# Kernel tuning notes

Hardware: AMD Instinct MI355X
Metric: run time of the kernel (lower is better)

The kernel has to match this reference:

```python
import jax, jax.numpy as jnp
import numpy as np

COST_CLASS = 1.0
COST_BBOX = 1.0
COST_GIOU = 1.0


def box_cxcywh_to_xyxy(b):
    cx, cy, w, h = jnp.split(b, 4, axis=-1)
    return jnp.concatenate([cx - 0.5 * w, cy - 0.5 * h, cx + 0.5 * w, cy + 0.5 * h], axis=-1)


def generalized_box_iou(b1, b2):
    # b1: [N,4] xyxy, b2: [M,4] xyxy -> [N,M]
    a1 = (b1[:, 2] - b1[:, 0]) * (b1[:, 3] - b1[:, 1])  # [N]
    a2 = (b2[:, 2] - b2[:, 0]) * (b2[:, 3] - b2[:, 1])  # [M]
    lt = jnp.maximum(b1[:, None, :2], b2[None, :, :2])  # [N,M,2]
    rb = jnp.minimum(b1[:, None, 2:], b2[None, :, 2:])
    wh = jnp.clip(rb - lt, 0.0)
    inter = wh[..., 0] * wh[..., 1]
    union = a1[:, None] + a2[None, :] - inter
    iou = inter / union
    lt_e = jnp.minimum(b1[:, None, :2], b2[None, :, :2])
    rb_e = jnp.maximum(b1[:, None, 2:], b2[None, :, 2:])
    wh_e = jnp.clip(rb_e - lt_e, 0.0)
    area = wh_e[..., 0] * wh_e[..., 1]
    return iou - (area - union) / area


def setup_inputs() -> dict:
    key = jax.random.key(0)
    k1, k2, k3, k4, k5 = jax.random.split(key, 5)
    bs, nq, d, total_tgt = 16, 900, 256, 1600
    return {
        "pred_logits": jax.random.normal(k1, (bs, nq, d), dtype=jnp.float32),
        "pred_boxes": jax.random.uniform(k2, (bs, nq, 4), dtype=jnp.float32),
        "tgt_embs": jax.random.normal(k3, (total_tgt, d), dtype=jnp.float32),
        "tgt_bbox": jax.random.uniform(k4, (total_tgt, 4), dtype=jnp.float32),
        "tgt_sizes": jax.random.randint(k5, (bs,), 0, 100, dtype=jnp.int32),  # only used by host-side LSA
    }


def reference(pred_logits, pred_boxes, tgt_embs, tgt_bbox, tgt_sizes):
    # Returns the sigmoid-squashed cost volume C [bs, num_queries, total_tgt];
    # scipy linear_sum_assignment over tgt_sizes splits is a host-side step.
    bs, nq = pred_logits.shape[:2]
    out_prob = pred_logits.reshape(bs * nq, -1)
    out_bbox = pred_boxes.reshape(bs * nq, 4)
    out_prob = out_prob / jnp.linalg.norm(out_prob, axis=-1, keepdims=True)
    cost_class = jax.nn.relu(out_prob @ tgt_embs.T)                    # [N,M]
    cost_bbox = jnp.sum(jnp.abs(out_bbox[:, None, :] - tgt_bbox[None, :, :]), axis=-1)  # L1 cdist
    cost_giou = -generalized_box_iou(box_cxcywh_to_xyxy(out_bbox), box_cxcywh_to_xyxy(tgt_bbox))
    C = COST_BBOX * cost_bbox + COST_CLASS * cost_class + COST_GIOU * cost_giou
    return jax.nn.sigmoid(C.reshape(bs, nq, -1))
```

## Files before the change

### kernel.cpp

```cpp
#include <hip/hip_runtime.h>

#define N_ROWS 14400
#define M_COLS 1600
#define KDIM   256
#define GRID_X 25
#define GRID_Y 225
#define NWG    (GRID_X * GRID_Y)

typedef __attribute__((ext_vector_type(8))) short bf16x8;
typedef __attribute__((ext_vector_type(4))) float f32x4;

__device__ __forceinline__ short f2bf(float x) {
  union { float f; unsigned u; } v; v.f = x;
  unsigned r = v.u + 0x7FFFu + ((v.u >> 16) & 1u);
  return (short)(r >> 16);
}

__device__ __forceinline__ void gload_lds16(const void* g, void* l) {
  __builtin_amdgcn_global_load_lds(
      (const __attribute__((address_space(1))) void*)g,
      (__attribute__((address_space(3))) void*)l, 16, 0, 0);
}

__global__ __launch_bounds__(256) void prep_kernel(
    const float* __restrict__ logits, const float* __restrict__ embs,
    short* __restrict__ probB, short* __restrict__ embB) {
  const int row = blockIdx.x * 4 + (threadIdx.x >> 6);
  const int lane = threadIdx.x & 63;
  if (row < N_ROWS) {
    const float4 x = ((const float4*)(logits + (size_t)row * KDIM))[lane];
    float s = x.x * x.x + x.y * x.y + x.z * x.z + x.w * x.w;
#pragma unroll
    for (int o = 32; o > 0; o >>= 1) s += __shfl_xor(s, o, 64);
    const float scale = __builtin_amdgcn_rsqf(s);
    short4 o4;
    o4.x = f2bf(x.x * scale); o4.y = f2bf(x.y * scale);
    o4.z = f2bf(x.z * scale); o4.w = f2bf(x.w * scale);
    ((short4*)(probB + (size_t)row * KDIM))[lane] = o4;
  } else {
    const int r = row - N_ROWS;
    const float4 x = ((const float4*)(embs + (size_t)r * KDIM))[lane];
    short4 o4;
    o4.x = f2bf(x.x); o4.y = f2bf(x.y); o4.z = f2bf(x.z); o4.w = f2bf(x.w);
    ((short4*)(embB + (size_t)r * KDIM))[lane] = o4;
  }
}

__global__ __launch_bounds__(256) void cost_kernel(
    const short* __restrict__ probB, const short* __restrict__ embB,
    const float* __restrict__ pbox, const float* __restrict__ tbox,
    float* __restrict__ out) {
  __shared__ short AB[2][64 * 64];
  __shared__ f32x4 rowcc[64], rowxy[64];
  __shared__ f32x4 colcc[64], colxy[64];
  short* const As = AB[0];
  short* const Bs = AB[1];
  float* const tbuf = (float*)AB;

  const int t = threadIdx.x;
  const int lane = t & 63;
  const int wid = t >> 6;
  const int wr = wid >> 1;
  const int wc = wid & 1;

  const int orig = blockIdx.x;
  const int xcd = orig & 7;
  const int rem = orig >> 3;
  const int q = NWG >> 3, r = NWG & 7;
  const int wgid = (xcd < r ? xcd * (q + 1) : r * (q + 1) + (xcd - r) * q) + rem;
  const int bx = wgid % GRID_X;
  const int by = wgid / GRID_X;
  const int rowBase = by * 64;
  const int colBase = bx * 64;

  if (t < 64) {
    const float4 bb = ((const float4*)pbox)[rowBase + t];
    rowcc[t] = (f32x4){bb.x, bb.y, bb.z, bb.w};
    rowxy[t] = (f32x4){fmaf(-0.5f, bb.z, bb.x), fmaf(-0.5f, bb.w, bb.y),
                       fmaf(0.5f, bb.z, bb.x), fmaf(0.5f, bb.w, bb.y)};
  } else if (t < 128) {
    const int c = t - 64;
    const float4 bb = ((const float4*)tbox)[colBase + c];
    colcc[c] = (f32x4){bb.x, bb.y, bb.z, bb.w};
    colxy[c] = (f32x4){fmaf(-0.5f, bb.z, bb.x), fmaf(-0.5f, bb.w, bb.y),
                       fmaf(0.5f, bb.z, bb.x), fmaf(0.5f, bb.w, bb.y)};
  }

  f32x4 acc[2][2];
#pragma unroll
  for (int i = 0; i < 2; ++i)
#pragma unroll
    for (int j = 0; j < 2; ++j) acc[i][j] = (f32x4){0.f, 0.f, 0.f, 0.f};

  const int swz = (lane & 7) ^ (lane >> 3);
  const int rbase = wid * 8 + (lane >> 3);

  for (int kt = 0; kt < 4; ++kt) {
    const int k0 = kt * 64 + swz * 8;
#pragma unroll
    for (int i = 0; i < 2; ++i) {
      const int gr = rowBase + i * 32 + rbase;
      gload_lds16(probB + (size_t)gr * KDIM + k0, As + (i * 32 + wid * 8) * 64);
    }
#pragma unroll
    for (int i = 0; i < 2; ++i) {
      const int gc = colBase + i * 32 + rbase;
      gload_lds16(embB + (size_t)gc * KDIM + k0, Bs + (i * 32 + wid * 8) * 64);
    }
    __syncthreads();
#pragma unroll
    for (int kk = 0; kk < 2; ++kk) {
      bf16x8 af[2], bfr[2];
      const int g = kk * 4 + (lane >> 4);
#pragma unroll
      for (int mi = 0; mi < 2; ++mi) {
        const int row = wr * 32 + mi * 16 + (lane & 15);
        af[mi] = *(const bf16x8*)(As + row * 64 + ((g ^ (row & 7)) * 8));
      }
#pragma unroll
      for (int ni = 0; ni < 2; ++ni) {
        const int row = wc * 32 + ni * 16 + (lane & 15);
        bfr[ni] = *(const bf16x8*)(Bs + row * 64 + ((g ^ (row & 7)) * 8));
      }
#pragma unroll
      for (int mi = 0; mi < 2; ++mi)
#pragma unroll
        for (int ni = 0; ni < 2; ++ni)
          acc[mi][ni] = __builtin_amdgcn_mfma_f32_16x16x32_bf16(
              af[mi], bfr[ni], acc[mi][ni], 0, 0, 0);
    }
    __syncthreads();
  }

  const float LOG2E = 1.44269504f;
  const int jr = (lane >> 4) * 4;
  const int lc = lane & 15;
  f32x4 c0v[2], c1v[2];
  float cav[2];
#pragma unroll
  for (int ni = 0; ni < 2; ++ni) {
    const int cloc = wc * 32 + ni * 16 + lc;
    c0v[ni] = colcc[cloc];
    c1v[ni] = colxy[cloc];
    cav[ni] = c0v[ni][2] * c0v[ni][3];
  }

#pragma unroll
  for (int mi = 0; mi < 2; ++mi) {
#pragma unroll
    for (int j = 0; j < 4; ++j) {
      const int row = wr * 32 + mi * 16 + jr + j;
      const f32x4 r0 = rowcc[row];
      const f32x4 r1 = rowxy[row];
      const float ra = r0[2] * r0[3];
      const int cswz = ((row >> 2) & 3) << 4;
#pragma unroll
      for (int ni = 0; ni < 2; ++ni) {
        const f32x4 c0 = c0v[ni], c1 = c1v[ni];
        const float cc = fmaxf(acc[mi][ni][j], 0.0f);
        const float l1 = fabsf(r0[0] - c0[0]) + fabsf(r0[1] - c0[1]) +
                         fabsf(r0[2] - c0[2]) + fabsf(r0[3] - c0[3]);
        const float iwx = fminf(r1[2], c1[2]) - fmaxf(r1[0], c1[0]);
        const float iwy = fminf(r1[3], c1[3]) - fmaxf(r1[1], c1[1]);
        const float iw = fmaxf(iwx, 0.f);
        const float ih = fmaxf(iwy, 0.f);
        const float inter = iw * ih;
        const float uni = ra + cav[ni] - inter;
        const float ex = (r0[2] + c0[2]) - iwx;
        const float ey = (r0[3] + c0[3]) - iwy;
        const float earea = ex * ey;
        const float num = fmaf(uni, uni, inter * earea);
        const float Cv = fmaf(-num, __builtin_amdgcn_rcpf(uni * earea),
                              l1 + cc + 1.0f);
        const float sg = __builtin_amdgcn_rcpf(
            1.0f + __builtin_amdgcn_exp2f(-LOG2E * Cv));
        const int col = wc * 32 + ni * 16 + lc;
        tbuf[row * 64 + (col ^ cswz)] = sg;
      }
    }
  }
  asm volatile("s_waitcnt lgkmcnt(0)" ::: "memory");
  __builtin_amdgcn_s_barrier();
#pragma unroll
  for (int rr = 0; rr < 4; ++rr) {
    const int row = rr * 16 + (t >> 4);
    const int col = (t & 15) * 4;
    const int cswz = ((row >> 2) & 3) << 4;
    const f32x4 v = *(const f32x4*)(tbuf + row * 64 + (col ^ cswz));
    __builtin_nontemporal_store(
        v, (f32x4*)(out + (size_t)(rowBase + row) * M_COLS + colBase + col));
  }
}

extern "C" void kernel_launch(void* const* d_in, const int* in_sizes, int n_in,
                              void* d_out, int out_size, void* d_ws, size_t ws_size,
                              hipStream_t stream) {
  const float* logits = (const float*)d_in[0];
  const float* pbox   = (const float*)d_in[1];
  const float* embs   = (const float*)d_in[2];
  const float* tbox   = (const float*)d_in[3];
  float* out = (float*)d_out;

  short* probB = (short*)d_ws;
  short* embB  = probB + (size_t)N_ROWS * KDIM;

  prep_kernel<<<(N_ROWS + M_COLS) / 4, 256, 0, stream>>>(logits, embs, probB, embB);

  cost_kernel<<<NWG, 256, 0, stream>>>(probB, embB, pbox, tbox, out);
}
```

Baseline: 49.04 us.

## Load full K panel into LDS once, removing per-k-tile barriers

The cost kernel now stages the whole 64x256 A and B bf16 panels into LDS with one batch of async global-to-LDS loads and a single barrier, instead of four k-tiles each separated by two barriers. This puts all global loads in flight together and removes six synchronisations per workgroup. The epilogue staging buffer switches from an XOR-swizzled layout to a padded row stride of 68. In exchange LDS use grows from about 16KB to about 64KB per workgroup, which can reduce the number of resident workgroups per CU and therefore latency hiding.

Result: slower. 60.22 us (+22.8%).

```diff
diff --git a/kernel.cpp b/kernel.cpp
--- a/kernel.cpp
+++ b/kernel.cpp
@@ -50,12 +50,11 @@
     const short* __restrict__ probB, const short* __restrict__ embB,
     const float* __restrict__ pbox, const float* __restrict__ tbox,
     float* __restrict__ out) {
-  __shared__ short AB[2][64 * 64];
+  __shared__ short As[64 * 256];
+  __shared__ short Bs[64 * 256];
   __shared__ f32x4 rowcc[64], rowxy[64];
   __shared__ f32x4 colcc[64], colxy[64];
-  short* const As = AB[0];
-  short* const Bs = AB[1];
-  float* const tbuf = (float*)AB;
+  float* const tbuf = (float*)As;
 
   const int t = threadIdx.x;
   const int lane = t & 63;
@@ -92,45 +91,49 @@
 #pragma unroll
     for (int j = 0; j < 2; ++j) acc[i][j] = (f32x4){0.f, 0.f, 0.f, 0.f};
 
-  const int swz = (lane & 7) ^ (lane >> 3);
-  const int rbase = wid * 8 + (lane >> 3);
-
-  for (int kt = 0; kt < 4; ++kt) {
-    const int k0 = kt * 64 + swz * 8;
-#pragma unroll
-    for (int i = 0; i < 2; ++i) {
-      const int gr = rowBase + i * 32 + rbase;
-      gload_lds16(probB + (size_t)gr * KDIM + k0, As + (i * 32 + wid * 8) * 64);
-    }
-#pragma unroll
-    for (int i = 0; i < 2; ++i) {
-      const int gc = colBase + i * 32 + rbase;
-      gload_lds16(embB + (size_t)gc * KDIM + k0, Bs + (i * 32 + wid * 8) * 64);
-    }
-    __syncthreads();
-#pragma unroll
-    for (int kk = 0; kk < 2; ++kk) {
-      bf16x8 af[2], bfr[2];
-      const int g = kk * 4 + (lane >> 4);
-#pragma unroll
-      for (int mi = 0; mi < 2; ++mi) {
-        const int row = wr * 32 + mi * 16 + (lane & 15);
-        af[mi] = *(const bf16x8*)(As + row * 64 + ((g ^ (row & 7)) * 8));
-      }
-#pragma unroll
-      for (int ni = 0; ni < 2; ++ni) {
-        const int row = wc * 32 + ni * 16 + (lane & 15);
-        bfr[ni] = *(const bf16x8*)(Bs + row * 64 + ((g ^ (row & 7)) * 8));
-      }
-#pragma unroll
-      for (int mi = 0; mi < 2; ++mi)
-#pragma unroll
-        for (int ni = 0; ni < 2; ++ni)
-          acc[mi][ni] = __builtin_amdgcn_mfma_f32_16x16x32_bf16(
-              af[mi], bfr[ni], acc[mi][ni], 0, 0, 0);
-    }
-    __syncthreads();
-  }
+  {
+    const int lrow = lane >> 5;
+    const int lgran = lane & 31;
+#pragma unroll
+    for (int ri = 0; ri < 8; ++ri) {
+      const int rloc = ri * 8 + wid * 2 + lrow;
+      const int gsrc = lgran ^ (rloc & 7);
+      gload_lds16(probB + (size_t)(rowBase + rloc) * KDIM + gsrc * 8,
+                  As + (ri * 8 + wid * 2) * 256);
+    }
+#pragma unroll
+    for (int ri = 0; ri < 8; ++ri) {
+      const int rloc = ri * 8 + wid * 2 + lrow;
+      const int gsrc = lgran ^ (rloc & 7);
+      gload_lds16(embB + (size_t)(colBase + rloc) * KDIM + gsrc * 8,
+                  Bs + (ri * 8 + wid * 2) * 256);
+    }
+  }
+  __syncthreads();
+
+#pragma unroll 2
+  for (int kk = 0; kk < 8; ++kk) {
+    bf16x8 af[2], bfr[2];
+    const int g = kk * 4 + (lane >> 4);
+#pragma unroll
+    for (int mi = 0; mi < 2; ++mi) {
+      const int row = wr * 32 + mi * 16 + (lane & 15);
+      af[mi] = *(const bf16x8*)(As + row * 256 + ((g ^ (row & 7)) * 8));
+    }
+#pragma unroll
+    for (int ni = 0; ni < 2; ++ni) {
+      const int row = wc * 32 + ni * 16 + (lane & 15);
+      bfr[ni] = *(const bf16x8*)(Bs + row * 256 + ((g ^ (row & 7)) * 8));
+    }
+#pragma unroll
+    for (int mi = 0; mi < 2; ++mi)
+#pragma unroll
+      for (int ni = 0; ni < 2; ++ni)
+        acc[mi][ni] = __builtin_amdgcn_mfma_f32_16x16x32_bf16(
+            af[mi], bfr[ni], acc[mi][ni], 0, 0, 0);
+  }
+  asm volatile("s_waitcnt lgkmcnt(0)" ::: "memory");
+  __builtin_amdgcn_s_barrier();
 
   const float LOG2E = 1.44269504f;
   const int jr = (lane >> 4) * 4;
@@ -153,7 +156,6 @@
       const f32x4 r0 = rowcc[row];
       const f32x4 r1 = rowxy[row];
       const float ra = r0[2] * r0[3];
-      const int cswz = ((row >> 2) & 3) << 4;
 #pragma unroll
       for (int ni = 0; ni < 2; ++ni) {
         const f32x4 c0 = c0v[ni], c1 = c1v[ni];
@@ -174,8 +176,7 @@
                               l1 + cc + 1.0f);
         const float sg = __builtin_amdgcn_rcpf(
             1.0f + __builtin_amdgcn_exp2f(-LOG2E * Cv));
-        const int col = wc * 32 + ni * 16 + lc;
-        tbuf[row * 64 + (col ^ cswz)] = sg;
+        tbuf[row * 68 + wc * 32 + ni * 16 + lc] = sg;
       }
     }
   }
@@ -185,8 +186,7 @@
   for (int rr = 0; rr < 4; ++rr) {
     const int row = rr * 16 + (t >> 4);
     const int col = (t & 15) * 4;
-    const int cswz = ((row >> 2) & 3) << 4;
-    const f32x4 v = *(const f32x4*)(tbuf + row * 64 + (col ^ cswz));
+    const f32x4 v = *(const f32x4*)(tbuf + row * 68 + col);
     __builtin_nontemporal_store(
         v, (f32x4*)(out + (size_t)(rowBase + row) * M_COLS + colBase + col));
   }
```
